# Optimization experiments

Measured on AMD Instinct MI355X. Metric: run time of the kernel, lower is better.

## Reference

```python
import jax, jax.numpy as jnp
import numpy as np

T, E, H, V, K = 1024, 300, 512, 100000, 12
START, STOP = 10, 11


def setup_inputs() -> dict:
    key = jax.random.key(0)
    ks = jax.random.split(key, 12)
    s = 0.05
    sentence = jax.random.randint(ks[0], (T,), 0, V, dtype=jnp.int32)
    tags = jax.random.randint(ks[1], (T,), 0, START, dtype=jnp.int32)  # real tags only
    word_embeds = jax.random.normal(ks[2], (V, E), jnp.float32) * 0.1

    def lstm_p(k):
        k1, k2 = jax.random.split(k)
        return (jax.random.normal(k1, (4 * H, E), jnp.float32) * s,
                jax.random.normal(k2, (4 * H, H), jnp.float32) * s,
                jnp.zeros(4 * H, jnp.float32), jnp.zeros(4 * H, jnp.float32))

    Wih_f, Whh_f, bih_f, bhh_f = lstm_p(ks[3])
    Wih_b, Whh_b, bih_b, bhh_b = lstm_p(ks[4])
    D = 2 * H
    attn_W = jax.random.normal(ks[5], (D, D), jnp.float32) * s
    attn_b = jnp.zeros(D, jnp.float32)
    h2h1_W = jax.random.normal(ks[6], (D, 2 * D), jnp.float32) * s
    h2h1_b = jnp.zeros(D, jnp.float32)
    tag_W = jax.random.normal(ks[7], (K, D), jnp.float32) * s
    tag_b = jnp.zeros(K, jnp.float32)
    transitions = jax.random.normal(ks[8], (K, K), jnp.float32) * 0.01
    transitions = transitions.at[START, :].set(-10000.0).at[:, STOP].set(-10000.0)
    return dict(sentence=sentence, tags=tags, word_embeds=word_embeds,
                Wih_f=Wih_f, Whh_f=Whh_f, bih_f=bih_f, bhh_f=bhh_f,
                Wih_b=Wih_b, Whh_b=Whh_b, bih_b=bih_b, bhh_b=bhh_b,
                attn_W=attn_W, attn_b=attn_b, h2h1_W=h2h1_W, h2h1_b=h2h1_b,
                tag_W=tag_W, tag_b=tag_b, transitions=transitions)


def _lstm_pass(x, Wih, Whh, bih, bhh):
    # x: [T, E] -> hs: [T, H]   (PyTorch LSTM gate order i,f,g,o)
    xg = x @ Wih.T + bih  # [T, 4H] precomputed input contribution

    def step(carry, g_in):
        h, c = carry
        g = g_in + h @ Whh.T + bhh
        i, f, gg, o = jnp.split(g, 4)
        i = jax.nn.sigmoid(i); f = jax.nn.sigmoid(f)
        gg = jnp.tanh(gg); o = jax.nn.sigmoid(o)
        c = f * c + i * gg
        h = o * jnp.tanh(c)
        return (h, c), h

    init = (jnp.zeros(H, x.dtype), jnp.zeros(H, x.dtype))
    _, hs = jax.lax.scan(step, init, xg)
    return hs


def reference(sentence, tags, word_embeds, Wih_f, Whh_f, bih_f, bhh_f,
              Wih_b, Whh_b, bih_b, bhh_b, attn_W, attn_b,
              h2h1_W, h2h1_b, tag_W, tag_b, transitions):
    x = word_embeds[sentence]                       # [T, E]  (dropout is eval no-op)
    h_fwd = _lstm_pass(x, Wih_f, Whh_f, bih_f, bhh_f)
    h_bwd = _lstm_pass(x[::-1], Wih_b, Whh_b, bih_b, bhh_b)[::-1]
    enc = jnp.concatenate([h_fwd, h_bwd], axis=-1)  # [T, 2H]

    # Attn 'general': energy(t, i) = enc[t] . (W enc[i] + b); vectorized per-timestep loop
    proj = enc @ attn_W.T + attn_b                  # [T, 2H]
    scores = enc @ proj.T                           # [T, T]
    w = jax.nn.softmax(scores, axis=-1)
    ctx = w @ enc                                   # [T, 2H]

    h1 = jnp.tanh(jnp.concatenate([enc, ctx], axis=-1) @ h2h1_W.T + h2h1_b)  # [T, 2H]
    feats = h1 @ tag_W.T + tag_b                    # [T, K]

    # CRF forward algorithm (log partition); transitions[to, from]
    alpha0 = jnp.full((K,), -10000.0, feats.dtype).at[START].set(0.0)

    def crf_step(alpha, feat):
        a = jax.nn.logsumexp(alpha[None, :] + transitions, axis=1) + feat
        return a, None

    alpha, _ = jax.lax.scan(crf_step, alpha0, feats)
    logZ = jax.nn.logsumexp(alpha + transitions[STOP])

    # gold path score (_score_sentence)
    pad_start = jnp.concatenate([jnp.array([START], tags.dtype), tags])
    pad_stop = jnp.concatenate([tags, jnp.array([STOP], tags.dtype)])
    gold = transitions[pad_stop, pad_start].sum() + feats[jnp.arange(T), tags].sum()

    return logZ - gold  # CRF negative log-likelihood for this sentence
```

## Files before the change

### kernel.cpp

```cpp
#include <hip/hip_runtime.h>
#include <hip/hip_fp16.h>

#define T_LEN 1024
#define E_DIM 300
#define H_DIM 512
#define D_DIM 1024
#define K_TAGS 12
#define G4 2048

typedef __attribute__((ext_vector_type(8))) short short8x;
typedef __attribute__((ext_vector_type(4))) float f32x4;

static __device__ __forceinline__ float frcp(float x){ return __builtin_amdgcn_rcpf(x); }
static __device__ __forceinline__ float sigm(float x){ return frcp(1.f + __expf(-x)); }
static __device__ __forceinline__ float ftanh(float x){
  const float e = __expf(2.f * fabsf(x));
  const float t = 1.f - 2.f * frcp(e + 1.f);
  return copysignf(t, x);
}
static __device__ __forceinline__ unsigned short f2b(float f){
  unsigned u = __float_as_uint(f);
  return (unsigned short)((u + 0x7fffu + ((u >> 16) & 1u)) >> 16);
}
static __device__ __forceinline__ uint4 pack8(const float* s){
  uint4 o;
  o.x = (unsigned)f2b(s[0]) | ((unsigned)f2b(s[1]) << 16);
  o.y = (unsigned)f2b(s[2]) | ((unsigned)f2b(s[3]) << 16);
  o.z = (unsigned)f2b(s[4]) | ((unsigned)f2b(s[5]) << 16);
  o.w = (unsigned)f2b(s[6]) | ((unsigned)f2b(s[7]) << 16);
  return o;
}

__global__ void k_gather(const int* __restrict__ sent, const float* __restrict__ we,
                         float* __restrict__ x){
  int idx = blockIdx.x*256 + threadIdx.x;
  if (idx < T_LEN*E_DIM){
    int t = idx / E_DIM, e = idx - t*E_DIM;
    x[idx] = we[(size_t)sent[t]*E_DIM + e];
  }
}

__global__ void k_init(unsigned* __restrict__ hbuf){
  int i = blockIdx.x*256 + threadIdx.x;
  if (i < 2048) hbuf[i] = 0u;
}

__global__ __launch_bounds__(256) void k_gemm_mfma(
    const float* __restrict__ Af, int lda, int arev,
    const float* __restrict__ Bf, const unsigned short* __restrict__ Bh, int ldb,
    const float* __restrict__ bias, int act,
    float* __restrict__ C, int ldc, int M, int N, int K)
{
  __shared__ __align__(16) unsigned short As[64*40];
  __shared__ __align__(16) unsigned short Bs[64*40];
  const int tid = threadIdx.x;
  const int bm = blockIdx.y*64, bn = blockIdx.x*64;
  const int r  = tid >> 2, c8 = (tid & 3) * 8;
  const int wave = tid >> 6, lane = tid & 63;
  const int wm = (wave >> 1) * 32, wn = (wave & 1) * 32;
  const int col = lane & 15, quad = lane >> 4;

  const int am = arev ? (M-1-(bm+r)) : (bm+r);
  const float* arow = Af + (size_t)am*lda;
  const float* brow = Bf ? (Bf + (size_t)(bn+r)*ldb) : (const float*)0;
  const unsigned short* brh = Bh ? (Bh + (size_t)(bn+r)*ldb) : (const unsigned short*)0;

  uint4* aw = (uint4*)(As + r*40 + c8);
  uint4* bw = (uint4*)(Bs + r*40 + c8);

  f32x4 acc[2][2];
  #pragma unroll
  for (int i=0;i<2;i++)
    #pragma unroll
    for (int j=0;j<2;j++) acc[i][j] = (f32x4){0.f,0.f,0.f,0.f};

  for (int k0 = 0; k0 < K; k0 += 32){
    uint4 avv, bvv;
    if (k0 + 32 <= K){
      avv = pack8(arow + k0 + c8);
      bvv = Bh ? *(const uint4*)(brh + k0 + c8) : pack8(brow + k0 + c8);
    } else {
      float ta[8], tb[8];
      #pragma unroll
      for (int i=0;i<8;i++){
        const int kk = k0 + c8 + i;
        ta[i] = (kk < K) ? arow[kk] : 0.f;
        tb[i] = (kk < K && Bf) ? brow[kk] : 0.f;
      }
      avv = pack8(ta); bvv = pack8(tb);
    }
    if (k0) __syncthreads();
    *aw = avv; *bw = bvv;
    __syncthreads();
    const short8x a0 = *(const short8x*)(As + (wm+col)*40    + quad*8);
    const short8x a1 = *(const short8x*)(As + (wm+16+col)*40 + quad*8);
    const short8x b0 = *(const short8x*)(Bs + (wn+col)*40    + quad*8);
    const short8x b1 = *(const short8x*)(Bs + (wn+16+col)*40 + quad*8);
    acc[0][0] = __builtin_amdgcn_mfma_f32_16x16x32_bf16(a0, b0, acc[0][0], 0, 0, 0);
    acc[0][1] = __builtin_amdgcn_mfma_f32_16x16x32_bf16(a0, b1, acc[0][1], 0, 0, 0);
    acc[1][0] = __builtin_amdgcn_mfma_f32_16x16x32_bf16(a1, b0, acc[1][0], 0, 0, 0);
    acc[1][1] = __builtin_amdgcn_mfma_f32_16x16x32_bf16(a1, b1, acc[1][1], 0, 0, 0);
  }

  #pragma unroll
  for (int mt=0;mt<2;mt++){
    #pragma unroll
    for (int nt=0;nt<2;nt++){
      const int cc = bn + wn + 16*nt + col;
      const float bs = bias ? bias[cc] : 0.f;
      #pragma unroll
      for (int i=0;i<4;i++){
        const int rr = bm + wm + 16*mt + quad*4 + i;
        float v = acc[mt][nt][i] + bs;
        if (act) v = ftanh(v);
        C[(size_t)rr*ldc + cc] = v;
      }
    }
  }
}

__global__ __launch_bounds__(256, 1) void k_lstm(
    const float* __restrict__ Whh_f, const float* __restrict__ Whh_b,
    const float* __restrict__ bih_f, const float* __restrict__ bhh_f,
    const float* __restrict__ bih_b, const float* __restrict__ bhh_b,
    const float* __restrict__ xg_f, const float* __restrict__ xg_b,
    unsigned* __restrict__ hbuf, float* __restrict__ enc)
{
  const int dir = blockIdx.x >> 5;
  const int w   = blockIdx.x & 31;
  const int tid = threadIdx.x;
  const int wave = tid >> 6, lane = tid & 63;
  const int col = lane & 15, quad = lane >> 4;

  const float* Whh = dir ? Whh_b : Whh_f;
  const float* xg  = dir ? xg_b  : xg_f;

  const int rowA = wave*H_DIM + w*16 + col;
  short8x w_frag[16];
  #pragma unroll
  for (int s=0;s<16;s++){
    const float* bp = Whh + (size_t)rowA*H_DIM + s*32 + quad*8;
    uint4 u = pack8(bp);
    w_frag[s] = *reinterpret_cast<short8x*>(&u);
  }

  float bias_r = 0.f, xg_cur = 0.f, c_reg = 0.f;
  int row2 = 0;
  if (tid < 64){
    row2 = (tid >> 4)*H_DIM + w*16 + (tid & 15);
    bias_r = dir ? (bih_b[row2] + bhh_b[row2]) : (bih_f[row2] + bhh_f[row2]);
    xg_cur = xg[row2];
  }

  __shared__ __align__(16) unsigned short lds_hb[512];
  __shared__ __align__(16) float raw[64];

  unsigned* hb = hbuf + dir*1024;

  for (int t = 1; t <= T_LEN; ++t){
    {
      unsigned* s0 = hb + ((t-1)&1)*512 + tid;
      const unsigned want = (unsigned)(t-1);
      unsigned v0 = __hip_atomic_load(s0,     __ATOMIC_RELAXED, __HIP_MEMORY_SCOPE_AGENT);
      unsigned v1 = __hip_atomic_load(s0+256, __ATOMIC_RELAXED, __HIP_MEMORY_SCOPE_AGENT);
      while (((v0 >> 16) != want) || ((v1 >> 16) != want)){
        v0 = __hip_atomic_load(s0,     __ATOMIC_RELAXED, __HIP_MEMORY_SCOPE_AGENT);
        v1 = __hip_atomic_load(s0+256, __ATOMIC_RELAXED, __HIP_MEMORY_SCOPE_AGENT);
      }
      lds_hb[tid]     = (unsigned short)(v0 & 0xffffu);
      lds_hb[tid+256] = (unsigned short)(v1 & 0xffffu);
    }
    __syncthreads();

    float xg_nxt = 0.f;
    if (tid < 64 && t < T_LEN) xg_nxt = xg[(size_t)t*G4 + row2];

    f32x4 a0 = (f32x4){0.f,0.f,0.f,0.f}, a1 = (f32x4){0.f,0.f,0.f,0.f};
    #pragma unroll
    for (int s=0;s<16;s+=2){
      const short8x b0 = *(const short8x*)(lds_hb + s*32     + quad*8);
      const short8x b1 = *(const short8x*)(lds_hb + (s+1)*32 + quad*8);
      a0 = __builtin_amdgcn_mfma_f32_16x16x32_bf16(w_frag[s],   b0, a0, 0, 0, 0);
      a1 = __builtin_amdgcn_mfma_f32_16x16x32_bf16(w_frag[s+1], b1, a1, 0, 0, 0);
    }
    if (col == 0){
      f32x4 asum = a0 + a1;
      *reinterpret_cast<f32x4*>(raw + wave*16 + quad*4) = asum;
    }
    __syncthreads();

    if (tid < 64){
      float v = raw[tid] + bias_r + xg_cur;
      const float va = ((tid >> 4) == 2) ? ftanh(v) : sigm(v);
      const int l2 = tid & 15;
      const float iv = __shfl(va, l2);
      const float fv = __shfl(va, l2 + 16);
      const float gg = __shfl(va, l2 + 32);
      const float ov = __shfl(va, l2 + 48);
      if (tid < 16){
        c_reg = fv*c_reg + iv*gg;
        const float hh = ov*ftanh(c_reg);
        const int hj = w*16 + tid;
        const unsigned hv = ((unsigned)t << 16) | (unsigned)f2b(hh);
        __hip_atomic_store(hb + (t&1)*512 + hj, hv,
                           __ATOMIC_RELAXED, __HIP_MEMORY_SCOPE_AGENT);
        const int tt = dir ? (T_LEN - t) : (t - 1);
        enc[(size_t)tt*D_DIM + dir*H_DIM + hj] = hh;
      }
      xg_cur = xg_nxt;
    }
    __syncthreads();
  }
}

__global__ __launch_bounds__(256) void k_softmax(float* __restrict__ S){
  float* r = S + (size_t)blockIdx.x*1024;
  const int tid = threadIdx.x;
  float v[4];
  #pragma unroll
  for (int i=0;i<4;i++) v[i] = r[tid + i*256];
  float m = fmaxf(fmaxf(v[0],v[1]), fmaxf(v[2],v[3]));
  #pragma unroll
  for (int off=32; off>=1; off>>=1) m = fmaxf(m, __shfl_xor(m, off));
  __shared__ float red[4], red2[4];
  const int wid = tid >> 6, lane = tid & 63;
  if (lane == 0) red[wid] = m;
  __syncthreads();
  m = fmaxf(fmaxf(red[0],red[1]), fmaxf(red[2],red[3]));
  float s = 0.f;
  #pragma unroll
  for (int i=0;i<4;i++){ v[i] = __expf(v[i]-m); s += v[i]; }
  #pragma unroll
  for (int off=32; off>=1; off>>=1) s += __shfl_xor(s, off);
  if (lane == 0) red2[wid] = s;
  __syncthreads();
  s = red2[0]+red2[1]+red2[2]+red2[3];
  const float inv = frcp(s);
  #pragma unroll
  for (int i=0;i<4;i++) r[tid + i*256] = v[i]*inv;
}

__global__ void k_copy_enc(const float* __restrict__ enc, float* __restrict__ cat){
  int idx = blockIdx.x*256 + threadIdx.x;
  if (idx < T_LEN*D_DIM){
    int t = idx >> 10, d = idx & 1023;
    cat[(size_t)t*2048 + d] = enc[idx];
  }
}

__global__ __launch_bounds__(256) void k_castT(const float* __restrict__ src,
                                               unsigned short* __restrict__ dst){
  __shared__ float tile[32][33];
  const int bx = blockIdx.x*32, by = blockIdx.y*32;
  const int tx = threadIdx.x & 31, ty8 = threadIdx.x >> 5;
  #pragma unroll
  for (int i=ty8;i<32;i+=8) tile[i][tx] = src[(size_t)(by+i)*1024 + bx+tx];
  __syncthreads();
  #pragma unroll
  for (int i=ty8;i<32;i+=8) dst[(size_t)(bx+i)*1024 + by+tx] = f2b(tile[tx][i]);
}

__global__ __launch_bounds__(256) void k_feats(
    const float* __restrict__ h1, const float* __restrict__ tagW,
    const float* __restrict__ tagb, float* __restrict__ feats)
{
  const int t = blockIdx.x;
  const int wave = threadIdx.x >> 6, lane = threadIdx.x & 63;
  const float* hr = h1 + (size_t)t*D_DIM;
  float hv[16];
  #pragma unroll
  for (int i=0;i<16;i++) hv[i] = hr[lane + 64*i];
  #pragma unroll
  for (int j=0;j<3;j++){
    const int tag = wave*3 + j;
    const float* wr = tagW + (size_t)tag*D_DIM;
    float s = 0.f;
    #pragma unroll
    for (int i=0;i<16;i++) s += hv[i]*wr[lane + 64*i];
    #pragma unroll
    for (int off=32; off>=1; off>>=1) s += __shfl_xor(s, off);
    if (lane == 0) feats[(size_t)t*K_TAGS + tag] = s + tagb[tag];
  }
}

__global__ __launch_bounds__(64) void k_crf1(const float* __restrict__ feats,
                                             const float* __restrict__ trans,
                                             float* __restrict__ chunkM){
  const int c = blockIdx.x;
  const int r = threadIdx.x;
  __shared__ float sT[144];
  __shared__ float sF[16*12];
  for (int i=r; i<144; i+=64) sT[i] = trans[i];
  const int t0 = c*16;
  for (int i=r; i<192; i+=64) sF[i] = feats[(size_t)t0*K_TAGS + i];
  __syncthreads();
  if (r < 12){
    float m[12], nm[12];
    #pragma unroll
    for (int k=0;k<12;k++) m[k] = sT[k*12 + r] + sF[k];
    for (int s=1; s<16; ++s){
      #pragma unroll
      for (int i=0;i<12;i++){
        float v[12]; float mx = -1e30f;
        #pragma unroll
        for (int k=0;k<12;k++){ v[k] = sT[i*12+k] + m[k]; mx = fmaxf(mx, v[k]); }
        float ss = 0.f;
        #pragma unroll
        for (int k=0;k<12;k++) ss += __expf(v[k]-mx);
        nm[i] = sF[s*12+i] + mx + __logf(ss);
      }
      #pragma unroll
      for (int i=0;i<12;i++) m[i] = nm[i];
    }
    #pragma unroll
    for (int k=0;k<12;k++) chunkM[c*144 + k*12 + r] = m[k];
  }
}

__global__ __launch_bounds__(128) void k_crf2(const float* __restrict__ chunkM,
                                              const float* __restrict__ feats,
                                              const float* __restrict__ trans,
                                              const int* __restrict__ tags,
                                              float* __restrict__ out){
  const int tid = threadIdx.x, wave = tid >> 6, lane = tid & 63;
  __shared__ float sGold;
  float alpha = (lane == 10) ? 0.f : -10000.f;
  if (wave == 1){
    float g = 0.f;
    for (int i = lane; i <= T_LEN; i += 64){
      const int to = (i < T_LEN) ? tags[i]   : 11;
      const int fr = (i == 0)    ? 10        : tags[i-1];
      g += trans[to*K_TAGS + fr];
      if (i < T_LEN) g += feats[(size_t)i*K_TAGS + tags[i]];
    }
    #pragma unroll
    for (int off=32; off>=1; off>>=1) g += __shfl_xor(g, off);
    if (lane == 0) sGold = g;
  } else {
    float pf[12];
    #pragma unroll
    for (int k=0;k<12;k++) pf[k] = (lane < 12) ? chunkM[lane*12 + k] : 0.f;
    for (int c=0; c<64; ++c){
      float av[12];
      #pragma unroll
      for (int j=0;j<12;j++) av[j] = __shfl(alpha, j);
      float cur[12];
      #pragma unroll
      for (int k=0;k<12;k++) cur[k] = pf[k];
      if (c+1 < 64){
        #pragma unroll
        for (int k=0;k<12;k++)
          pf[k] = (lane < 12) ? chunkM[(c+1)*144 + lane*12 + k] : 0.f;
      }
      if (lane < 12){
        float v[12]; float mx = -1e30f;
        #pragma unroll
        for (int k=0;k<12;k++){ v[k] = cur[k] + av[k]; mx = fmaxf(mx, v[k]); }
        float ss = 0.f;
        #pragma unroll
        for (int k=0;k<12;k++) ss += __expf(v[k]-mx);
        alpha = mx + __logf(ss);
      }
    }
  }
  __syncthreads();
  if (wave == 0){
    float v = (lane < K_TAGS) ? (alpha + trans[11*K_TAGS + lane]) : -1e30f;
    float m = v;
    #pragma unroll
    for (int off=32; off>=1; off>>=1) m = fmaxf(m, __shfl_xor(m, off));
    float e = (lane < K_TAGS) ? __expf(v - m) : 0.f;
    #pragma unroll
    for (int off=32; off>=1; off>>=1) e += __shfl_xor(e, off);
    if (lane == 0) out[0] = (m + __logf(e)) - sGold;
  }
}

extern "C" void kernel_launch(void* const* d_in, const int* in_sizes, int n_in,
                              void* d_out, int out_size, void* d_ws, size_t ws_size,
                              hipStream_t stream)
{
  const int*   sentence = (const int*)d_in[0];
  const int*   tags     = (const int*)d_in[1];
  const float* we       = (const float*)d_in[2];
  const float* Wih_f    = (const float*)d_in[3];
  const float* Whh_f    = (const float*)d_in[4];
  const float* bih_f    = (const float*)d_in[5];
  const float* bhh_f    = (const float*)d_in[6];
  const float* Wih_b    = (const float*)d_in[7];
  const float* Whh_b    = (const float*)d_in[8];
  const float* bih_b    = (const float*)d_in[9];
  const float* bhh_b    = (const float*)d_in[10];
  const float* attn_W   = (const float*)d_in[11];
  const float* attn_b   = (const float*)d_in[12];
  const float* h2h1_W   = (const float*)d_in[13];
  const float* h2h1_b   = (const float*)d_in[14];
  const float* tag_W    = (const float*)d_in[15];
  const float* tag_b    = (const float*)d_in[16];
  const float* trans    = (const float*)d_in[17];
  float* out = (float*)d_out;

  float* ws     = (float*)d_ws;
  float* cat    = ws;
  float* reg2   = cat  + 2097152;
  float* enc    = reg2 + 2097152;
  float* proj   = enc  + 1048576;
  float* feats  = proj + 1048576;
  unsigned* hbuf= (unsigned*)(feats + 12288);
  float* xg_f   = cat;
  float* xg_b   = reg2;
  float* scores = reg2;
  float* h1     = reg2 + 1048576;
  float* x      = proj;
  unsigned short* encT = (unsigned short*)proj;
  float* chunkM = proj + 524288;

  k_gather<<<dim3((T_LEN*E_DIM + 255)/256), dim3(256), 0, stream>>>(sentence, we, x);
  k_init<<<dim3(8), dim3(256), 0, stream>>>(hbuf);
  k_gemm_mfma<<<dim3(32,16), dim3(256), 0, stream>>>(x, E_DIM, 0,
      Wih_f, nullptr, E_DIM, nullptr, 0, xg_f, G4, T_LEN, G4, E_DIM);
  k_gemm_mfma<<<dim3(32,16), dim3(256), 0, stream>>>(x, E_DIM, 1,
      Wih_b, nullptr, E_DIM, nullptr, 0, xg_b, G4, T_LEN, G4, E_DIM);
  k_lstm<<<dim3(64), dim3(256), 0, stream>>>(Whh_f, Whh_b, bih_f, bhh_f,
      bih_b, bhh_b, xg_f, xg_b, hbuf, enc);
  k_gemm_mfma<<<dim3(16,16), dim3(256), 0, stream>>>(enc, D_DIM, 0,
      attn_W, nullptr, D_DIM, attn_b, 0, proj, D_DIM, T_LEN, D_DIM, D_DIM);
  k_gemm_mfma<<<dim3(16,16), dim3(256), 0, stream>>>(enc, D_DIM, 0,
      proj, nullptr, D_DIM, nullptr, 0, scores, T_LEN, T_LEN, T_LEN, D_DIM);
  k_softmax<<<dim3(1024), dim3(256), 0, stream>>>(scores);
  k_copy_enc<<<dim3(4096), dim3(256), 0, stream>>>(enc, cat);
  k_castT<<<dim3(32,32), dim3(256), 0, stream>>>(enc, encT);
  k_gemm_mfma<<<dim3(16,16), dim3(256), 0, stream>>>(scores, T_LEN, 0,
      nullptr, encT, D_DIM, nullptr, 0, cat + 1024, 2048, T_LEN, D_DIM, T_LEN);
  k_gemm_mfma<<<dim3(16,16), dim3(256), 0, stream>>>(cat, 2048, 0,
      h2h1_W, nullptr, 2048, h2h1_b, 1, h1, D_DIM, T_LEN, D_DIM, 2048);
  k_feats<<<dim3(1024), dim3(256), 0, stream>>>(h1, tag_W, tag_b, feats);
  k_crf1<<<dim3(64), dim3(64), 0, stream>>>(feats, trans, chunkM);
  k_crf2<<<dim3(1), dim3(128), 0, stream>>>(chunkM, feats, trans, tags, out);
}
```

Measured before the change: 1.859 ms.

## Pre-cast GEMM operands to bf16 and feed GEMMs raw bf16 tiles

Result: faster. 1.790 ms (-3.7%).

```diff
diff --git a/kernel.cpp b/kernel.cpp
--- a/kernel.cpp
+++ b/kernel.cpp
@@ -30,13 +30,34 @@
   o.w = (unsigned)f2b(s[6]) | ((unsigned)f2b(s[7]) << 16);
   return o;
 }
+static __device__ __forceinline__ uint4 pack8u(const unsigned short* s){
+  uint4 o;
+  o.x = (unsigned)s[0] | ((unsigned)s[1] << 16);
+  o.y = (unsigned)s[2] | ((unsigned)s[3] << 16);
+  o.z = (unsigned)s[4] | ((unsigned)s[5] << 16);
+  o.w = (unsigned)s[6] | ((unsigned)s[7] << 16);
+  return o;
+}
 
 __global__ void k_gather(const int* __restrict__ sent, const float* __restrict__ we,
-                         float* __restrict__ x){
+                         unsigned short* __restrict__ xh){
   int idx = blockIdx.x*256 + threadIdx.x;
   if (idx < T_LEN*E_DIM){
     int t = idx / E_DIM, e = idx - t*E_DIM;
-    x[idx] = we[(size_t)sent[t]*E_DIM + e];
+    xh[idx] = f2b(we[(size_t)sent[t]*E_DIM + e]);
+  }
+}
+
+__global__ __launch_bounds__(256) void k_cast(const float* __restrict__ src,
+                                              unsigned short* __restrict__ dst,
+                                              int n4){
+  int i = blockIdx.x*256 + threadIdx.x;
+  if (i < n4){
+    const float4 v = *reinterpret_cast<const float4*>(src + (size_t)i*4);
+    ushort2 a, b;
+    a.x = f2b(v.x); a.y = f2b(v.y); b.x = f2b(v.z); b.y = f2b(v.w);
+    *reinterpret_cast<ushort2*>(dst + (size_t)i*4)     = a;
+    *reinterpret_cast<ushort2*>(dst + (size_t)i*4 + 2) = b;
   }
 }
 
@@ -46,10 +67,10 @@
 }
 
 __global__ __launch_bounds__(256) void k_gemm_mfma(
-    const float* __restrict__ Af, int lda, int arev,
-    const float* __restrict__ Bf, const unsigned short* __restrict__ Bh, int ldb,
+    const unsigned short* __restrict__ Ah, int lda, int arev,
+    const unsigned short* __restrict__ Bh, int ldb,
     const float* __restrict__ bias, int act,
-    float* __restrict__ C, int ldc, int M, int N, int K)
+    void* __restrict__ Cp, int ldc, int cbf16, int M, int N, int K)
 {
   __shared__ __align__(16) unsigned short As[64*40];
   __shared__ __align__(16) unsigned short Bs[64*40];
@@ -61,9 +82,8 @@
   const int col = lane & 15, quad = lane >> 4;
 
   const int am = arev ? (M-1-(bm+r)) : (bm+r);
-  const float* arow = Af + (size_t)am*lda;
-  const float* brow = Bf ? (Bf + (size_t)(bn+r)*ldb) : (const float*)0;
-  const unsigned short* brh = Bh ? (Bh + (size_t)(bn+r)*ldb) : (const unsigned short*)0;
+  const unsigned short* arow = Ah + (size_t)am*lda;
+  const unsigned short* brow = Bh + (size_t)(bn+r)*ldb;
 
   uint4* aw = (uint4*)(As + r*40 + c8);
   uint4* bw = (uint4*)(Bs + r*40 + c8);
@@ -77,17 +97,17 @@
   for (int k0 = 0; k0 < K; k0 += 32){
     uint4 avv, bvv;
     if (k0 + 32 <= K){
-      avv = pack8(arow + k0 + c8);
-      bvv = Bh ? *(const uint4*)(brh + k0 + c8) : pack8(brow + k0 + c8);
+      avv = *(const uint4*)(arow + k0 + c8);
+      bvv = *(const uint4*)(brow + k0 + c8);
     } else {
-      float ta[8], tb[8];
+      unsigned short ta[8], tb[8];
       #pragma unroll
       for (int i=0;i<8;i++){
         const int kk = k0 + c8 + i;
-        ta[i] = (kk < K) ? arow[kk] : 0.f;
-        tb[i] = (kk < K && Bf) ? brow[kk] : 0.f;
-      }
-      avv = pack8(ta); bvv = pack8(tb);
+        ta[i] = (kk < K) ? arow[kk] : (unsigned short)0;
+        tb[i] = (kk < K) ? brow[kk] : (unsigned short)0;
+      }
+      avv = pack8u(ta); bvv = pack8u(tb);
     }
     if (k0) __syncthreads();
     *aw = avv; *bw = bvv;
@@ -113,7 +133,8 @@
         const int rr = bm + wm + 16*mt + quad*4 + i;
         float v = acc[mt][nt][i] + bs;
         if (act) v = ftanh(v);
-        C[(size_t)rr*ldc + cc] = v;
+        if (cbf16) ((unsigned short*)Cp)[(size_t)rr*ldc + cc] = f2b(v);
+        else       ((float*)Cp)[(size_t)rr*ldc + cc] = v;
       }
     }
   }
@@ -213,8 +234,10 @@
   }
 }
 
-__global__ __launch_bounds__(256) void k_softmax(float* __restrict__ S){
+__global__ __launch_bounds__(256) void k_softmax(float* __restrict__ S,
+                                                 unsigned short* __restrict__ Sh){
   float* r = S + (size_t)blockIdx.x*1024;
+  unsigned short* rh = Sh + (size_t)blockIdx.x*1024;
   const int tid = threadIdx.x;
   float v[4];
   #pragma unroll
@@ -237,14 +260,19 @@
   s = red2[0]+red2[1]+red2[2]+red2[3];
   const float inv = frcp(s);
   #pragma unroll
-  for (int i=0;i<4;i++) r[tid + i*256] = v[i]*inv;
-}
-
-__global__ void k_copy_enc(const float* __restrict__ enc, float* __restrict__ cat){
+  for (int i=0;i<4;i++){
+    const float o = v[i]*inv;
+    r[tid + i*256]  = o;
+    rh[tid + i*256] = f2b(o);
+  }
+}
+
+__global__ void k_copy_enc(const float* __restrict__ enc,
+                           unsigned short* __restrict__ cath){
   int idx = blockIdx.x*256 + threadIdx.x;
   if (idx < T_LEN*D_DIM){
     int t = idx >> 10, d = idx & 1023;
-    cat[(size_t)t*2048 + d] = enc[idx];
+    cath[(size_t)t*2048 + d] = f2b(enc[idx]);
   }
 }
 
@@ -400,40 +428,53 @@
   const float* trans    = (const float*)d_in[17];
   float* out = (float*)d_out;
 
-  float* ws     = (float*)d_ws;
-  float* cat    = ws;
-  float* reg2   = cat  + 2097152;
-  float* enc    = reg2 + 2097152;
-  float* proj   = enc  + 1048576;
-  float* feats  = proj + 1048576;
-  unsigned* hbuf= (unsigned*)(feats + 12288);
-  float* xg_f   = cat;
-  float* xg_b   = reg2;
-  float* scores = reg2;
-  float* h1     = reg2 + 1048576;
-  float* x      = proj;
-  unsigned short* encT = (unsigned short*)proj;
-  float* chunkM = proj + 524288;
-
-  k_gather<<<dim3((T_LEN*E_DIM + 255)/256), dim3(256), 0, stream>>>(sentence, we, x);
+  float* ws = (float*)d_ws;
+  float* R1 = ws;
+  float* R2 = ws + 2097152;
+  float* R3 = ws + 4194304;
+  float* R4 = ws + 5242880;
+  float* feats = ws + 6291456;
+  unsigned* hbuf = (unsigned*)(ws + 6303744);
+
+  float* xg_f = R1;
+  float* xg_b = R2;
+  float* enc  = R3;
+  unsigned short* xh      = (unsigned short*)R4;
+  unsigned short* Wih_fh  = (unsigned short*)R4 + 307200;
+  unsigned short* Wih_bh  = (unsigned short*)R4 + 921600;
+  unsigned short* cath    = (unsigned short*)R1;
+  unsigned short* attn_Wh = (unsigned short*)(R1 + 1048576);
+  unsigned short* h2h1_Wh = (unsigned short*)R2;
+  float* scores = R2 + 1048576;
+  unsigned short* encT    = (unsigned short*)R4;
+  unsigned short* projh   = (unsigned short*)R4 + 1048576;
+  unsigned short* scoresh = (unsigned short*)R3;
+  float* h1     = R3;
+  float* chunkM = R4;
+
+  k_gather<<<dim3((T_LEN*E_DIM + 255)/256), dim3(256), 0, stream>>>(sentence, we, xh);
   k_init<<<dim3(8), dim3(256), 0, stream>>>(hbuf);
-  k_gemm_mfma<<<dim3(32,16), dim3(256), 0, stream>>>(x, E_DIM, 0,
-      Wih_f, nullptr, E_DIM, nullptr, 0, xg_f, G4, T_LEN, G4, E_DIM);
-  k_gemm_mfma<<<dim3(32,16), dim3(256), 0, stream>>>(x, E_DIM, 1,
-      Wih_b, nullptr, E_DIM, nullptr, 0, xg_b, G4, T_LEN, G4, E_DIM);
+  k_cast<<<dim3(600),  dim3(256), 0, stream>>>(Wih_f, Wih_fh, 153600);
+  k_cast<<<dim3(600),  dim3(256), 0, stream>>>(Wih_b, Wih_bh, 153600);
+  k_gemm_mfma<<<dim3(32,16), dim3(256), 0, stream>>>(xh, E_DIM, 0,
+      Wih_fh, E_DIM, nullptr, 0, xg_f, G4, 0, T_LEN, G4, E_DIM);
+  k_gemm_mfma<<<dim3(32,16), dim3(256), 0, stream>>>(xh, E_DIM, 1,
+      Wih_bh, E_DIM, nullptr, 0, xg_b, G4, 0, T_LEN, G4, E_DIM);
   k_lstm<<<dim3(64), dim3(256), 0, stream>>>(Whh_f, Whh_b, bih_f, bhh_f,
       bih_b, bhh_b, xg_f, xg_b, hbuf, enc);
-  k_gemm_mfma<<<dim3(16,16), dim3(256), 0, stream>>>(enc, D_DIM, 0,
-      attn_W, nullptr, D_DIM, attn_b, 0, proj, D_DIM, T_LEN, D_DIM, D_DIM);
-  k_gemm_mfma<<<dim3(16,16), dim3(256), 0, stream>>>(enc, D_DIM, 0,
-      proj, nullptr, D_DIM, nullptr, 0, scores, T_LEN, T_LEN, T_LEN, D_DIM);
-  k_softmax<<<dim3(1024), dim3(256), 0, stream>>>(scores);
-  k_copy_enc<<<dim3(4096), dim3(256), 0, stream>>>(enc, cat);
+  k_copy_enc<<<dim3(4096), dim3(256), 0, stream>>>(enc, cath);
   k_castT<<<dim3(32,32), dim3(256), 0, stream>>>(enc, encT);
-  k_gemm_mfma<<<dim3(16,16), dim3(256), 0, stream>>>(scores, T_LEN, 0,
-      nullptr, encT, D_DIM, nullptr, 0, cat + 1024, 2048, T_LEN, D_DIM, T_LEN);
-  k_gemm_mfma<<<dim3(16,16), dim3(256), 0, stream>>>(cat, 2048, 0,
-      h2h1_W, nullptr, 2048, h2h1_b, 1, h1, D_DIM, T_LEN, D_DIM, 2048);
+  k_cast<<<dim3(1024), dim3(256), 0, stream>>>(attn_W, attn_Wh, 262144);
+  k_cast<<<dim3(2048), dim3(256), 0, stream>>>(h2h1_W, h2h1_Wh, 524288);
+  k_gemm_mfma<<<dim3(16,16), dim3(256), 0, stream>>>(cath, 2048, 0,
+      attn_Wh, D_DIM, attn_b, 0, projh, D_DIM, 1, T_LEN, D_DIM, D_DIM);
+  k_gemm_mfma<<<dim3(16,16), dim3(256), 0, stream>>>(cath, 2048, 0,
+      projh, D_DIM, nullptr, 0, scores, T_LEN, 0, T_LEN, T_LEN, D_DIM);
+  k_softmax<<<dim3(1024), dim3(256), 0, stream>>>(scores, scoresh);
+  k_gemm_mfma<<<dim3(16,16), dim3(256), 0, stream>>>(scoresh, T_LEN, 0,
+      encT, D_DIM, nullptr, 0, cath + 1024, 2048, 1, T_LEN, D_DIM, T_LEN);
+  k_gemm_mfma<<<dim3(16,16), dim3(256), 0, stream>>>(cath, 2048, 0,
+      h2h1_Wh, 2048, h2h1_b, 1, h1, D_DIM, 0, T_LEN, D_DIM, 2048);
   k_feats<<<dim3(1024), dim3(256), 0, stream>>>(h1, tag_W, tag_b, feats);
   k_crf1<<<dim3(64), dim3(64), 0, stream>>>(feats, trans, chunkM);
   k_crf2<<<dim3(1), dim3(128), 0, stream>>>(chunkM, feats, trans, tags, out);
```
